# Optimization experiments

Hardware: AMD Instinct MI355X
Metric: run time of the kernel (lower is better)

## Reference

```python
import jax, jax.numpy as jnp
import numpy as np

HIDDEN = 512
N_HEAD = 8
D_HEAD = 64
MAX_REL = 3
B, S = 2, 2048


def setup_inputs() -> dict:
    key = jax.random.key(0)
    ks = jax.random.split(key, 12)
    sc = 1.0 / np.sqrt(HIDDEN)
    return {
        "query": jax.random.normal(ks[0], (B, S, HIDDEN), jnp.float32),
        "key_": jax.random.normal(ks[1], (B, S, HIDDEN), jnp.float32),
        "value": jax.random.normal(ks[2], (B, S, HIDDEN), jnp.float32),
        "mask": jnp.zeros((B, S, S), dtype=bool),
        "pos_matrix": jax.random.randint(ks[3], (S, S), 0, MAX_REL, jnp.int32),
        "Wq": jax.random.normal(ks[4], (HIDDEN, HIDDEN), jnp.float32) * sc,
        "bq": jnp.zeros((HIDDEN,), jnp.float32),
        "Wk": jax.random.normal(ks[5], (HIDDEN, HIDDEN), jnp.float32) * sc,
        "bk": jnp.zeros((HIDDEN,), jnp.float32),
        "Wv": jax.random.normal(ks[6], (HIDDEN, HIDDEN), jnp.float32) * sc,
        "bv": jnp.zeros((HIDDEN,), jnp.float32),
        "Wo": jax.random.normal(ks[7], (HIDDEN, HIDDEN), jnp.float32) * sc,
        "bo": jnp.zeros((HIDDEN,), jnp.float32),
        "rel_table": jax.random.normal(ks[8], (MAX_REL, D_HEAD), jnp.float32) * 0.1,
    }


def reference(query, key_, value, mask, pos_matrix, Wq, bq, Wk, bk, Wv, bv, Wo, bo, rel_table):
    b, s, hid = query.shape
    H, D = N_HEAD, D_HEAD
    q = (query @ Wq + bq).reshape(b, s, H, D)   # [B,S,H,D]
    k = (key_ @ Wk + bk).reshape(b, s, H, D)
    v = (value @ Wv + bv).reshape(b, s, H, D)
    rel = rel_table[pos_matrix[:s, :s]]          # [S,S,D]
    # attn1: content-content; attn2: q vs rel-pos; attn3: k(row) vs rel-pos
    attn1 = jnp.einsum('bihd,bjhd->bhij', q, k)
    attn2 = jnp.einsum('bihd,ijd->bhij', q, rel)
    attn3 = jnp.einsum('bihd,ijd->bhij', k, rel)
    scale = jnp.sqrt(jnp.asarray(D, query.dtype))
    attn = (attn1 + attn2 + attn3) / scale
    attn = jnp.where(mask[:, None, :, :], jnp.asarray(-1e9, attn.dtype), attn)
    attn = jax.nn.softmax(attn, axis=-1)         # dropout=0 (eval)
    x = jnp.einsum('bhij,bjhd->bihd', attn, v).reshape(b, s, hid)
    out = x @ Wo + bo
    return out, attn
```

## Files before the change

kernel.cpp:

```cpp
#include <hip/hip_runtime.h>
#include <math.h>

#define SEQ   2048
#define BATCH 2
#define NHEAD 8
#define HID   512
#define LG8   0.180336880f
#define MASKV -3.0e8f

typedef unsigned char  u8;
typedef unsigned short u16;
typedef short short8 __attribute__((ext_vector_type(8)));
typedef float f32x4  __attribute__((ext_vector_type(4)));

__device__ __forceinline__ u16 f2bf(float f) {
    unsigned u = __float_as_uint(f);
    u = (u + 0x7FFF + ((u >> 16) & 1)) >> 16;
    return (u16)u;
}
__device__ __forceinline__ float bf2f(u16 h) {
    return __uint_as_float(((unsigned)h) << 16);
}

__global__ __launch_bounds__(256) void gemm_bias_kernel(
    const float* __restrict__ A, const float* __restrict__ W,
    const float* __restrict__ bias, float* __restrict__ C, int M)
{
    __shared__ float As[16][68];
    __shared__ float Bs[16][64];
    const int tid = threadIdx.x;
    const int ty = tid >> 4, tx = tid & 15;
    const int row0 = blockIdx.x << 6;
    const int col0 = blockIdx.y << 6;
    const int am = tid >> 2, ak = (tid & 3) << 2;
    const int wk = tid >> 4, wn = (tid & 15) << 2;

    float acc[4][4] = {};
    for (int k0 = 0; k0 < HID; k0 += 16) {
        float4 a4 = *(const float4*)&A[(size_t)(row0 + am) * HID + k0 + ak];
        float4 w4 = *(const float4*)&W[(size_t)(k0 + wk) * HID + col0 + wn];
        __syncthreads();
        As[ak + 0][am] = a4.x; As[ak + 1][am] = a4.y;
        As[ak + 2][am] = a4.z; As[ak + 3][am] = a4.w;
        *(float4*)&Bs[wk][wn] = w4;
        __syncthreads();
        #pragma unroll
        for (int kk = 0; kk < 16; ++kk) {
            float4 a = *(const float4*)&As[kk][ty << 2];
            float4 w = *(const float4*)&Bs[kk][tx << 2];
            acc[0][0] += a.x * w.x; acc[0][1] += a.x * w.y; acc[0][2] += a.x * w.z; acc[0][3] += a.x * w.w;
            acc[1][0] += a.y * w.x; acc[1][1] += a.y * w.y; acc[1][2] += a.y * w.z; acc[1][3] += a.y * w.w;
            acc[2][0] += a.z * w.x; acc[2][1] += a.z * w.y; acc[2][2] += a.z * w.z; acc[2][3] += a.z * w.w;
            acc[3][0] += a.w * w.x; acc[3][1] += a.w * w.y; acc[3][2] += a.w * w.z; acc[3][3] += a.w * w.w;
        }
    }
    float4 bv = *(const float4*)&bias[col0 + (tx << 2)];
    #pragma unroll
    for (int i = 0; i < 4; ++i) {
        float4 o = { acc[i][0] + bv.x, acc[i][1] + bv.y, acc[i][2] + bv.z, acc[i][3] + bv.w };
        *(float4*)&C[(size_t)(row0 + (ty << 2) + i) * HID + col0 + (tx << 2)] = o;
    }
}

__global__ __launch_bounds__(256) void convert_qkv_kernel(
    const float* __restrict__ q, const float* __restrict__ k, const float* __restrict__ v,
    u16* __restrict__ qh, u16* __restrict__ ql,
    u16* __restrict__ kh, u16* __restrict__ kl, u16* __restrict__ vb)
{
    const size_t i = ((size_t)blockIdx.x * 256 + threadIdx.x) * 4;
    float4 qv = *(const float4*)&q[i];
    float4 kv = *(const float4*)&k[i];
    float4 vv = *(const float4*)&v[i];
    ushort4 oqh, oql, okh, okl, ovb;
    float s; u16 hh;
    s = qv.x * LG8; hh = f2bf(s); oqh.x = hh; oql.x = f2bf(s - bf2f(hh));
    s = qv.y * LG8; hh = f2bf(s); oqh.y = hh; oql.y = f2bf(s - bf2f(hh));
    s = qv.z * LG8; hh = f2bf(s); oqh.z = hh; oql.z = f2bf(s - bf2f(hh));
    s = qv.w * LG8; hh = f2bf(s); oqh.w = hh; oql.w = f2bf(s - bf2f(hh));
    s = kv.x;       hh = f2bf(s); okh.x = hh; okl.x = f2bf(s - bf2f(hh));
    s = kv.y;       hh = f2bf(s); okh.y = hh; okl.y = f2bf(s - bf2f(hh));
    s = kv.z;       hh = f2bf(s); okh.z = hh; okl.z = f2bf(s - bf2f(hh));
    s = kv.w;       hh = f2bf(s); okh.w = hh; okl.w = f2bf(s - bf2f(hh));
    ovb.x = f2bf(vv.x); ovb.y = f2bf(vv.y); ovb.z = f2bf(vv.z); ovb.w = f2bf(vv.w);
    *(ushort4*)&qh[i] = oqh; *(ushort4*)&ql[i] = oql;
    *(ushort4*)&kh[i] = okh; *(ushort4*)&kl[i] = okl;
    *(ushort4*)&vb[i] = ovb;
}

__global__ __launch_bounds__(256) void convert_pm_kernel(
    const int* __restrict__ pos, const u8* __restrict__ mask, u8* __restrict__ pm)
{
    const size_t s = ((size_t)blockIdx.x * 256 + threadIdx.x) * 4;
    int4  p = *(const int4*)&pos[s & (size_t)(SEQ * SEQ - 1)];
    uchar4 m = *(const uchar4*)&mask[s];
    uchar4 o;
    o.x = m.x ? (u8)3 : (u8)p.x;
    o.y = m.y ? (u8)3 : (u8)p.y;
    o.z = m.z ? (u8)3 : (u8)p.z;
    o.w = m.w ? (u8)3 : (u8)p.w;
    *(uchar4*)&pm[s] = o;
}

__global__ __launch_bounds__(256) void rel_dots_kernel(
    const float* __restrict__ q, const float* __restrict__ k,
    const float* __restrict__ rel_table, float* __restrict__ dqk)
{
    const int w = blockIdx.x * 4 + (threadIdx.x >> 6);
    const int lane = threadIdx.x & 63;
    const int h = w % NHEAD;
    const int is = w / NHEAD;
    const int b = is / SEQ;
    const int i = is % SEQ;
    const size_t base = (size_t)is * HID + h * 64 + lane;
    const float s = q[base] + k[base];
    float p0 = s * rel_table[lane];
    float p1 = s * rel_table[64 + lane];
    float p2 = s * rel_table[128 + lane];
    #pragma unroll
    for (int off = 32; off; off >>= 1) {
        p0 += __shfl_xor(p0, off);
        p1 += __shfl_xor(p1, off);
        p2 += __shfl_xor(p2, off);
    }
    if (lane == 0) {
        size_t o = (((size_t)b * NHEAD + h) * SEQ + i) << 2;
        dqk[o + 0] = p0 * LG8; dqk[o + 1] = p1 * LG8; dqk[o + 2] = p2 * LG8;
    }
}

__global__ __launch_bounds__(256) void attn_stats_kernel(
    const u16* __restrict__ qh, const u16* __restrict__ ql,
    const u16* __restrict__ kh, const u16* __restrict__ kl,
    const float* __restrict__ dqk, const u8* __restrict__ pm,
    float* __restrict__ invl)
{
    __shared__ __align__(16) u16 Kh[64 * 72];
    __shared__ __align__(16) u16 Kl[64 * 72];
    __shared__ __align__(16) u8  PM[64 * 64];
    __shared__ float Ds[64][4];
    const int tid = threadIdx.x;
    const int wave = tid >> 6, lane = tid & 63;
    const int quad = lane >> 4, l15 = lane & 15;
    const int b = blockIdx.z, h = blockIdx.y, i0 = blockIdx.x << 6;
    const size_t bh = (size_t)(b * NHEAD + h);

    {
        const int i = tid >> 2, r = tid & 3;
        Ds[i][r] = (r == 3) ? MASKV : dqk[((bh * SEQ + i0 + i) << 2) + r];
    }
    const int irow = (wave << 4) + l15;
    const size_t qbase = ((size_t)(b * SEQ + i0 + irow)) * HID + h * 64 + (quad << 3);
    const short8 aqh0 = *(const short8*)&qh[qbase];
    const short8 aqh1 = *(const short8*)&qh[qbase + 32];
    const short8 aql0 = *(const short8*)&ql[qbase];
    const short8 aql1 = *(const short8*)&ql[qbase + 32];

    float srow[4] = {0.f, 0.f, 0.f, 0.f};

    for (int jt = 0; jt < SEQ / 64; ++jt) {
        const int j0 = jt << 6;
        __syncthreads();
        {
            const int rr = tid >> 3, cc = (tid & 7) << 3;
            const size_t g = ((size_t)(b * SEQ + j0 + rr)) * HID + h * 64 + cc;
            *(short8*)&Kh[rr * 72 + cc] = *(const short8*)&kh[g];
            *(short8*)&Kl[rr * 72 + cc] = *(const short8*)&kl[g];
            const size_t g2 = g + (size_t)32 * HID;
            *(short8*)&Kh[(rr + 32) * 72 + cc] = *(const short8*)&kh[g2];
            *(short8*)&Kl[(rr + 32) * 72 + cc] = *(const short8*)&kl[g2];
        }
        {
            const int r = tid >> 2, c = (tid & 3) << 4;
            *(uint4*)&PM[r * 64 + c] =
                *(const uint4*)&pm[((size_t)b * SEQ + i0 + r) * SEQ + j0 + c];
        }
        __syncthreads();

        #pragma unroll
        for (int sub = 0; sub < 4; ++sub) {
            const int n = (sub << 4) + l15;
            const short8 bh0 = *(const short8*)&Kh[n * 72 + (quad << 3)];
            const short8 bh1 = *(const short8*)&Kh[n * 72 + 32 + (quad << 3)];
            const short8 bl0 = *(const short8*)&Kl[n * 72 + (quad << 3)];
            const short8 bl1 = *(const short8*)&Kl[n * 72 + 32 + (quad << 3)];
            f32x4 acc = {0.f, 0.f, 0.f, 0.f};
            acc = __builtin_amdgcn_mfma_f32_16x16x32_bf16(aqh0, bh0, acc, 0, 0, 0);
            acc = __builtin_amdgcn_mfma_f32_16x16x32_bf16(aqh1, bh1, acc, 0, 0, 0);
            acc = __builtin_amdgcn_mfma_f32_16x16x32_bf16(aql0, bh0, acc, 0, 0, 0);
            acc = __builtin_amdgcn_mfma_f32_16x16x32_bf16(aql1, bh1, acc, 0, 0, 0);
            acc = __builtin_amdgcn_mfma_f32_16x16x32_bf16(aqh0, bl0, acc, 0, 0, 0);
            acc = __builtin_amdgcn_mfma_f32_16x16x32_bf16(aqh1, bl1, acc, 0, 0, 0);
            #pragma unroll
            for (int r = 0; r < 4; ++r) {
                const int il = (wave << 4) + (quad << 2) + r;
                const u8 p = PM[il * 64 + (sub << 4) + l15];
                srow[r] += exp2f(acc[r] + Ds[il][p]);
            }
        }
    }
    #pragma unroll
    for (int r = 0; r < 4; ++r) {
        float s = srow[r];
        s += __shfl_xor(s, 1); s += __shfl_xor(s, 2);
        s += __shfl_xor(s, 4); s += __shfl_xor(s, 8);
        if (l15 == 0)
            invl[bh * SEQ + i0 + (wave << 4) + (quad << 2) + r] = 1.0f / s;
    }
}

__global__ __launch_bounds__(256) void attn_fused_kernel(
    const u16* __restrict__ qh, const u16* __restrict__ ql,
    const u16* __restrict__ kh, const u16* __restrict__ kl,
    const u16* __restrict__ vb, const float* __restrict__ dqk,
    const u8* __restrict__ pm, const float* __restrict__ invl,
    float* __restrict__ attn, float* __restrict__ x)
{
    __shared__ __align__(16) u16 Kh[64 * 72];
    __shared__ __align__(16) u16 Kl[64 * 72];
    __shared__ __align__(16) u16 VtT[64 * 72];
    __shared__ __align__(16) u16 Pst[4][16 * 72];
    __shared__ __align__(16) u8  PM[64 * 64];
    __shared__ float Ds[64][4];
    const int tid = threadIdx.x;
    const int wave = tid >> 6, lane = tid & 63;
    const int quad = lane >> 4, l15 = lane & 15;
    const int b = blockIdx.z, h = blockIdx.y, i0 = blockIdx.x << 6;
    const size_t bh = (size_t)(b * NHEAD + h);

    {
        const int i = tid >> 2, r = tid & 3;
        Ds[i][r] = (r == 3) ? MASKV : dqk[((bh * SEQ + i0 + i) << 2) + r];
    }
    float inv_r[4];
    #pragma unroll
    for (int r = 0; r < 4; ++r)
        inv_r[r] = invl[bh * SEQ + i0 + (wave << 4) + (quad << 2) + r];

    const int irow = (wave << 4) + l15;
    const size_t qbase = ((size_t)(b * SEQ + i0 + irow)) * HID + h * 64 + (quad << 3);
    const short8 aqh0 = *(const short8*)&qh[qbase];
    const short8 aqh1 = *(const short8*)&qh[qbase + 32];
    const short8 aql0 = *(const short8*)&ql[qbase];
    const short8 aql1 = *(const short8*)&ql[qbase + 32];

    f32x4 accX[4] = {{0.f,0.f,0.f,0.f},{0.f,0.f,0.f,0.f},{0.f,0.f,0.f,0.f},{0.f,0.f,0.f,0.f}};

    for (int jt = 0; jt < SEQ / 64; ++jt) {
        const int j0 = jt << 6;
        __syncthreads();
        {
            const int rr = tid >> 3, cc = (tid & 7) << 3;
            const size_t g = ((size_t)(b * SEQ + j0 + rr)) * HID + h * 64 + cc;
            *(short8*)&Kh[rr * 72 + cc] = *(const short8*)&kh[g];
            *(short8*)&Kl[rr * 72 + cc] = *(const short8*)&kl[g];
            const size_t g2 = g + (size_t)32 * HID;
            *(short8*)&Kh[(rr + 32) * 72 + cc] = *(const short8*)&kh[g2];
            *(short8*)&Kl[(rr + 32) * 72 + cc] = *(const short8*)&kl[g2];
        }
        {
            const int r = tid >> 2, c = (tid & 3) << 4;
            *(uint4*)&PM[r * 64 + c] =
                *(const uint4*)&pm[((size_t)b * SEQ + i0 + r) * SEQ + j0 + c];
        }
        {
            const int jr = tid & 63, d0 = (tid >> 6) << 4;
            const size_t g = ((size_t)(b * SEQ + j0 + jr)) * HID + h * 64 + d0;
            const short8 v0 = *(const short8*)&vb[g];
            const short8 v1 = *(const short8*)&vb[g + 8];
            #pragma unroll
            for (int e = 0; e < 8; ++e) {
                VtT[(d0 + e) * 72 + jr]     = (u16)v0[e];
                VtT[(d0 + 8 + e) * 72 + jr] = (u16)v1[e];
            }
        }
        __syncthreads();

        #pragma unroll
        for (int sub = 0; sub < 4; ++sub) {
            const int n = (sub << 4) + l15;
            const short8 bh0 = *(const short8*)&Kh[n * 72 + (quad << 3)];
            const short8 bh1 = *(const short8*)&Kh[n * 72 + 32 + (quad << 3)];
            const short8 bl0 = *(const short8*)&Kl[n * 72 + (quad << 3)];
            const short8 bl1 = *(const short8*)&Kl[n * 72 + 32 + (quad << 3)];
            f32x4 acc = {0.f, 0.f, 0.f, 0.f};
            acc = __builtin_amdgcn_mfma_f32_16x16x32_bf16(aqh0, bh0, acc, 0, 0, 0);
            acc = __builtin_amdgcn_mfma_f32_16x16x32_bf16(aqh1, bh1, acc, 0, 0, 0);
            acc = __builtin_amdgcn_mfma_f32_16x16x32_bf16(aql0, bh0, acc, 0, 0, 0);
            acc = __builtin_amdgcn_mfma_f32_16x16x32_bf16(aql1, bh1, acc, 0, 0, 0);
            acc = __builtin_amdgcn_mfma_f32_16x16x32_bf16(aqh0, bl0, acc, 0, 0, 0);
            acc = __builtin_amdgcn_mfma_f32_16x16x32_bf16(aqh1, bl1, acc, 0, 0, 0);
            #pragma unroll
            for (int r = 0; r < 4; ++r) {
                const int il = (wave << 4) + (quad << 2) + r;
                const u8 p = PM[il * 64 + (sub << 4) + l15];
                const float pr = exp2f(acc[r] + Ds[il][p]) * inv_r[r];
                attn[(bh * SEQ + i0 + il) * SEQ + j0 + (sub << 4) + l15] = pr;
                Pst[wave][((quad << 2) + r) * 72 + (sub << 4) + l15] = f2bf(pr);
            }
        }
        const short8 bp0 = *(const short8*)&Pst[wave][l15 * 72 + (quad << 3)];
        const short8 bp1 = *(const short8*)&Pst[wave][l15 * 72 + 32 + (quad << 3)];
        #pragma unroll
        for (int m = 0; m < 4; ++m) {
            const short8 av0 = *(const short8*)&VtT[((m << 4) + l15) * 72 + (quad << 3)];
            const short8 av1 = *(const short8*)&VtT[((m << 4) + l15) * 72 + 32 + (quad << 3)];
            accX[m] = __builtin_amdgcn_mfma_f32_16x16x32_bf16(av0, bp0, accX[m], 0, 0, 0);
            accX[m] = __builtin_amdgcn_mfma_f32_16x16x32_bf16(av1, bp1, accX[m], 0, 0, 0);
        }
    }
    const size_t xrow = ((size_t)(b * SEQ + i0 + (wave << 4) + l15)) * HID + h * 64;
    #pragma unroll
    for (int m = 0; m < 4; ++m) {
        *(f32x4*)&x[xrow + (m << 4) + (quad << 2)] = accX[m];
    }
}

extern "C" void kernel_launch(void* const* d_in, const int* in_sizes, int n_in,
                              void* d_out, int out_size, void* d_ws, size_t ws_size,
                              hipStream_t stream) {
    (void)in_sizes; (void)n_in; (void)out_size; (void)ws_size;
    const float* query = (const float*)d_in[0];
    const float* key_  = (const float*)d_in[1];
    const float* value = (const float*)d_in[2];
    const u8*    mask  = (const u8*)d_in[3];
    const int*   pos   = (const int*)d_in[4];
    const float* Wq = (const float*)d_in[5];
    const float* bq = (const float*)d_in[6];
    const float* Wk = (const float*)d_in[7];
    const float* bk = (const float*)d_in[8];
    const float* Wv = (const float*)d_in[9];
    const float* bv = (const float*)d_in[10];
    const float* Wo = (const float*)d_in[11];
    const float* bo = (const float*)d_in[12];
    const float* rel_table = (const float*)d_in[13];

    float* out  = (float*)d_out;
    float* attn = out + (size_t)BATCH * SEQ * HID;

    float* q_ws = (float*)d_ws;
    float* k_ws = q_ws + (size_t)2097152;
    float* v_ws = k_ws + (size_t)2097152;
    float* dqk  = v_ws + (size_t)2097152;
    float* invl = dqk + (size_t)131072;
    u16* qh = (u16*)(invl + 32768);
    u16* ql = qh + (size_t)2097152;
    u16* kh = ql + (size_t)2097152;
    u16* kl = kh + (size_t)2097152;
    u16* vb = kl + (size_t)2097152;
    u8*  pm = (u8*)(vb + (size_t)2097152);
    float* x_ws = q_ws;

    const dim3 blk(256);
    const int M = BATCH * SEQ;

    gemm_bias_kernel<<<dim3(M / 64, HID / 64), blk, 0, stream>>>(query, Wq, bq, q_ws, M);
    gemm_bias_kernel<<<dim3(M / 64, HID / 64), blk, 0, stream>>>(key_, Wk, bk, k_ws, M);
    gemm_bias_kernel<<<dim3(M / 64, HID / 64), blk, 0, stream>>>(value, Wv, bv, v_ws, M);
    rel_dots_kernel<<<dim3(BATCH * SEQ * NHEAD / 4), blk, 0, stream>>>(q_ws, k_ws, rel_table, dqk);
    convert_qkv_kernel<<<dim3(2048), blk, 0, stream>>>(q_ws, k_ws, v_ws, qh, ql, kh, kl, vb);
    convert_pm_kernel<<<dim3(8192), blk, 0, stream>>>(pos, mask, pm);
    attn_stats_kernel<<<dim3(SEQ / 64, NHEAD, BATCH), blk, 0, stream>>>(
        qh, ql, kh, kl, dqk, pm, invl);
    attn_fused_kernel<<<dim3(SEQ / 64, NHEAD, BATCH), blk, 0, stream>>>(
        qh, ql, kh, kl, vb, dqk, pm, invl, attn, x_ws);
    gemm_bias_kernel<<<dim3(M / 64, HID / 64), blk, 0, stream>>>(x_ws, Wo, bo, out, M);
}
```

Before: 673.0 us.

## Move projections to split-bf16 MFMA GEMMs and materialize exp scores for separate PV pass

The four fp32 SIMT projection GEMMs become MFMA GEMMs that use a hi/lo bf16 split of activations and pre-transposed weights, preceded by conversion kernels. The attention is split differently. The stats pass now also writes unnormalized bf16 exp scores to a full BxHxSxS workspace. A second pass reads those scores back, writes the normalized attn output and does PV with a pre-transposed V. This cuts redundant QK recomputation and moves GEMM work to matrix cores. In exchange it adds a large extra global write and read of the score matrix, extra conversion and transpose launches, and K loads that now come straight from global instead of LDS. The attn output is now computed from bf16-rounded exp values, which lowers its precision.

```diff
diff --git a/kernel.cpp b/kernel.cpp
--- a/kernel.cpp
+++ b/kernel.cpp
@@ -21,73 +21,62 @@
 __device__ __forceinline__ float bf2f(u16 h) {
     return __uint_as_float(((unsigned)h) << 16);
 }
-
-__global__ __launch_bounds__(256) void gemm_bias_kernel(
-    const float* __restrict__ A, const float* __restrict__ W,
-    const float* __restrict__ bias, float* __restrict__ C, int M)
-{
-    __shared__ float As[16][68];
-    __shared__ float Bs[16][64];
-    const int tid = threadIdx.x;
-    const int ty = tid >> 4, tx = tid & 15;
-    const int row0 = blockIdx.x << 6;
-    const int col0 = blockIdx.y << 6;
-    const int am = tid >> 2, ak = (tid & 3) << 2;
-    const int wk = tid >> 4, wn = (tid & 15) << 2;
-
-    float acc[4][4] = {};
-    for (int k0 = 0; k0 < HID; k0 += 16) {
-        float4 a4 = *(const float4*)&A[(size_t)(row0 + am) * HID + k0 + ak];
-        float4 w4 = *(const float4*)&W[(size_t)(k0 + wk) * HID + col0 + wn];
-        __syncthreads();
-        As[ak + 0][am] = a4.x; As[ak + 1][am] = a4.y;
-        As[ak + 2][am] = a4.z; As[ak + 3][am] = a4.w;
-        *(float4*)&Bs[wk][wn] = w4;
-        __syncthreads();
-        #pragma unroll
-        for (int kk = 0; kk < 16; ++kk) {
-            float4 a = *(const float4*)&As[kk][ty << 2];
-            float4 w = *(const float4*)&Bs[kk][tx << 2];
-            acc[0][0] += a.x * w.x; acc[0][1] += a.x * w.y; acc[0][2] += a.x * w.z; acc[0][3] += a.x * w.w;
-            acc[1][0] += a.y * w.x; acc[1][1] += a.y * w.y; acc[1][2] += a.y * w.z; acc[1][3] += a.y * w.w;
-            acc[2][0] += a.z * w.x; acc[2][1] += a.z * w.y; acc[2][2] += a.z * w.z; acc[2][3] += a.z * w.w;
-            acc[3][0] += a.w * w.x; acc[3][1] += a.w * w.y; acc[3][2] += a.w * w.z; acc[3][3] += a.w * w.w;
-        }
-    }
-    float4 bv = *(const float4*)&bias[col0 + (tx << 2)];
-    #pragma unroll
-    for (int i = 0; i < 4; ++i) {
-        float4 o = { acc[i][0] + bv.x, acc[i][1] + bv.y, acc[i][2] + bv.z, acc[i][3] + bv.w };
-        *(float4*)&C[(size_t)(row0 + (ty << 2) + i) * HID + col0 + (tx << 2)] = o;
-    }
-}
-
-__global__ __launch_bounds__(256) void convert_qkv_kernel(
+__device__ __forceinline__ void split2(float s, u16& h, u16& l) {
+    h = f2bf(s); l = f2bf(s - bf2f(h));
+}
+
+__global__ __launch_bounds__(256) void conv_act(
     const float* __restrict__ q, const float* __restrict__ k, const float* __restrict__ v,
-    u16* __restrict__ qh, u16* __restrict__ ql,
-    u16* __restrict__ kh, u16* __restrict__ kl, u16* __restrict__ vb)
+    u16* __restrict__ Qh, u16* __restrict__ Ql, u16* __restrict__ Kh, u16* __restrict__ Kl,
+    u16* __restrict__ Vh, u16* __restrict__ Vl)
 {
     const size_t i = ((size_t)blockIdx.x * 256 + threadIdx.x) * 4;
     float4 qv = *(const float4*)&q[i];
     float4 kv = *(const float4*)&k[i];
     float4 vv = *(const float4*)&v[i];
-    ushort4 oqh, oql, okh, okl, ovb;
-    float s; u16 hh;
-    s = qv.x * LG8; hh = f2bf(s); oqh.x = hh; oql.x = f2bf(s - bf2f(hh));
-    s = qv.y * LG8; hh = f2bf(s); oqh.y = hh; oql.y = f2bf(s - bf2f(hh));
-    s = qv.z * LG8; hh = f2bf(s); oqh.z = hh; oql.z = f2bf(s - bf2f(hh));
-    s = qv.w * LG8; hh = f2bf(s); oqh.w = hh; oql.w = f2bf(s - bf2f(hh));
-    s = kv.x;       hh = f2bf(s); okh.x = hh; okl.x = f2bf(s - bf2f(hh));
-    s = kv.y;       hh = f2bf(s); okh.y = hh; okl.y = f2bf(s - bf2f(hh));
-    s = kv.z;       hh = f2bf(s); okh.z = hh; okl.z = f2bf(s - bf2f(hh));
-    s = kv.w;       hh = f2bf(s); okh.w = hh; okl.w = f2bf(s - bf2f(hh));
-    ovb.x = f2bf(vv.x); ovb.y = f2bf(vv.y); ovb.z = f2bf(vv.z); ovb.w = f2bf(vv.w);
-    *(ushort4*)&qh[i] = oqh; *(ushort4*)&ql[i] = oql;
-    *(ushort4*)&kh[i] = okh; *(ushort4*)&kl[i] = okl;
-    *(ushort4*)&vb[i] = ovb;
-}
-
-__global__ __launch_bounds__(256) void convert_pm_kernel(
+    ushort4 a, b, c, d, e, f;
+    split2(qv.x, a.x, b.x); split2(qv.y, a.y, b.y); split2(qv.z, a.z, b.z); split2(qv.w, a.w, b.w);
+    split2(kv.x, c.x, d.x); split2(kv.y, c.y, d.y); split2(kv.z, c.z, d.z); split2(kv.w, c.w, d.w);
+    split2(vv.x, e.x, f.x); split2(vv.y, e.y, f.y); split2(vv.z, e.z, f.z); split2(vv.w, e.w, f.w);
+    *(ushort4*)&Qh[i] = a; *(ushort4*)&Ql[i] = b;
+    *(ushort4*)&Kh[i] = c; *(ushort4*)&Kl[i] = d;
+    *(ushort4*)&Vh[i] = e; *(ushort4*)&Vl[i] = f;
+}
+
+__global__ __launch_bounds__(256) void conv_w(
+    const float* __restrict__ W0, const float* __restrict__ W1,
+    const float* __restrict__ W2, const float* __restrict__ W3,
+    u16* __restrict__ wt)
+{
+    __shared__ float T[64][68];
+    const float* Wz = (blockIdx.z == 0) ? W0 : (blockIdx.z == 1) ? W1 : (blockIdx.z == 2) ? W2 : W3;
+    u16* wh = wt + (size_t)blockIdx.z * 2 * 262144;
+    u16* wl = wh + 262144;
+    const int t = threadIdx.x;
+    const int k0 = blockIdx.x << 6, n0 = blockIdx.y << 6;
+    {
+        const int r = t >> 2, c = (t & 3) << 4;
+        #pragma unroll
+        for (int cc = 0; cc < 16; cc += 4)
+            *(float4*)&T[r][c + cc] = *(const float4*)&Wz[(size_t)(k0 + r) * HID + n0 + c + cc];
+    }
+    __syncthreads();
+    {
+        const int n = t >> 2, kc = (t & 3) << 4;
+        short8 h0, l0, h1, l1;
+        #pragma unroll
+        for (int e = 0; e < 8; ++e) {
+            u16 hh, ll;
+            split2(T[kc + e][n], hh, ll);     h0[e] = (short)hh; l0[e] = (short)ll;
+            split2(T[kc + 8 + e][n], hh, ll); h1[e] = (short)hh; l1[e] = (short)ll;
+        }
+        const size_t o = (size_t)(n0 + n) * HID + k0 + kc;
+        *(short8*)&wh[o] = h0; *(short8*)&wh[o + 8] = h1;
+        *(short8*)&wl[o] = l0; *(short8*)&wl[o + 8] = l1;
+    }
+}
+
+__global__ __launch_bounds__(256) void conv_pm(
     const int* __restrict__ pos, const u8* __restrict__ mask, u8* __restrict__ pm)
 {
     const size_t s = ((size_t)blockIdx.x * 256 + threadIdx.x) * 4;
@@ -101,8 +90,84 @@
     *(uchar4*)&pm[s] = o;
 }
 
+template<int OMODE>
+__global__ __launch_bounds__(256) void gemm_mfma(
+    const u16* __restrict__ Ah, const u16* __restrict__ Al,
+    const u16* __restrict__ Wh, const u16* __restrict__ Wl,
+    const float* __restrict__ bias,
+    float* __restrict__ Cf, u16* __restrict__ Ch, u16* __restrict__ Cl)
+{
+    const int tid = threadIdx.x;
+    const int wave = tid >> 6, lane = tid & 63;
+    const int quad = lane >> 4, l15 = lane & 15;
+    const int row0 = blockIdx.x << 6, n0 = blockIdx.y << 6;
+    const size_t abase = (size_t)(row0 + (wave << 4) + l15) * HID + (quad << 3);
+
+    f32x4 acc[4] = {{0.f,0.f,0.f,0.f},{0.f,0.f,0.f,0.f},{0.f,0.f,0.f,0.f},{0.f,0.f,0.f,0.f}};
+    #pragma unroll 4
+    for (int k0 = 0; k0 < HID; k0 += 32) {
+        const short8 ah = *(const short8*)&Ah[abase + k0];
+        const short8 al = *(const short8*)&Al[abase + k0];
+        #pragma unroll
+        for (int nt = 0; nt < 4; ++nt) {
+            const size_t wb = (size_t)(n0 + (nt << 4) + l15) * HID + k0 + (quad << 3);
+            const short8 bh = *(const short8*)&Wh[wb];
+            const short8 bl = *(const short8*)&Wl[wb];
+            acc[nt] = __builtin_amdgcn_mfma_f32_16x16x32_bf16(ah, bh, acc[nt], 0, 0, 0);
+            acc[nt] = __builtin_amdgcn_mfma_f32_16x16x32_bf16(al, bh, acc[nt], 0, 0, 0);
+            acc[nt] = __builtin_amdgcn_mfma_f32_16x16x32_bf16(ah, bl, acc[nt], 0, 0, 0);
+        }
+    }
+    #pragma unroll
+    for (int nt = 0; nt < 4; ++nt) {
+        const int col = n0 + (nt << 4) + l15;
+        const float bv = bias[col];
+        #pragma unroll
+        for (int r = 0; r < 4; ++r) {
+            const size_t idx = (size_t)(row0 + (wave << 4) + (quad << 2) + r) * HID + col;
+            const float v = acc[nt][r] + bv;
+            if (OMODE == 0) {
+                Cf[idx] = v;
+            } else if (OMODE == 1) {
+                u16 hh, ll; split2(v, hh, ll);
+                Ch[idx] = hh; Cl[idx] = ll;
+            } else {
+                Ch[idx] = f2bf(v);
+            }
+        }
+    }
+}
+
+__global__ __launch_bounds__(256) void transpose_v(
+    const u16* __restrict__ vb, u16* __restrict__ vt)
+{
+    __shared__ u16 T[64][72];
+    const int t = threadIdx.x;
+    const int j0 = blockIdx.x << 6, bhh = blockIdx.y;
+    const int b = bhh >> 3, h = bhh & 7;
+    {
+        const int r = t >> 2, c = (t & 3) << 4;
+        const size_t g = (size_t)(b * SEQ + j0 + r) * HID + h * 64 + c;
+        *(short8*)&T[r][c]     = *(const short8*)&vb[g];
+        *(short8*)&T[r][c + 8] = *(const short8*)&vb[g + 8];
+    }
+    __syncthreads();
+    {
+        const int d = t >> 2, jc = (t & 3) << 4;
+        short8 o0, o1;
+        #pragma unroll
+        for (int e = 0; e < 8; ++e) {
+            o0[e] = (short)T[jc + e][d];
+            o1[e] = (short)T[jc + 8 + e][d];
+        }
+        const size_t o = ((size_t)bhh * 64 + d) * SEQ + j0 + jc;
+        *(short8*)&vt[o] = o0; *(short8*)&vt[o + 8] = o1;
+    }
+}
+
 __global__ __launch_bounds__(256) void rel_dots_kernel(
-    const float* __restrict__ q, const float* __restrict__ k,
+    const u16* __restrict__ qh, const u16* __restrict__ ql,
+    const u16* __restrict__ kh, const u16* __restrict__ kl,
     const float* __restrict__ rel_table, float* __restrict__ dqk)
 {
     const int w = blockIdx.x * 4 + (threadIdx.x >> 6);
@@ -112,7 +177,7 @@
     const int b = is / SEQ;
     const int i = is % SEQ;
     const size_t base = (size_t)is * HID + h * 64 + lane;
-    const float s = q[base] + k[base];
+    const float s = (bf2f(qh[base]) + bf2f(ql[base])) + (bf2f(kh[base]) + bf2f(kl[base]));
     float p0 = s * rel_table[lane];
     float p1 = s * rel_table[64 + lane];
     float p2 = s * rel_table[128 + lane];
@@ -128,16 +193,14 @@
     }
 }
 
-__global__ __launch_bounds__(256) void attn_stats_kernel(
+__global__ __launch_bounds__(256) void attn_exp(
     const u16* __restrict__ qh, const u16* __restrict__ ql,
     const u16* __restrict__ kh, const u16* __restrict__ kl,
     const float* __restrict__ dqk, const u8* __restrict__ pm,
-    float* __restrict__ invl)
-{
-    __shared__ __align__(16) u16 Kh[64 * 72];
-    __shared__ __align__(16) u16 Kl[64 * 72];
-    __shared__ __align__(16) u8  PM[64 * 64];
+    u16* __restrict__ Pt, float* __restrict__ invl)
+{
     __shared__ float Ds[64][4];
+    __shared__ __align__(16) u16 Pst[4][16 * 72];
     const int tid = threadIdx.x;
     const int wave = tid >> 6, lane = tid & 63;
     const int quad = lane >> 4, l15 = lane & 15;
@@ -148,41 +211,26 @@
         const int i = tid >> 2, r = tid & 3;
         Ds[i][r] = (r == 3) ? MASKV : dqk[((bh * SEQ + i0 + i) << 2) + r];
     }
-    const int irow = (wave << 4) + l15;
-    const size_t qbase = ((size_t)(b * SEQ + i0 + irow)) * HID + h * 64 + (quad << 3);
+    __syncthreads();
+
+    const size_t qbase = ((size_t)(b * SEQ + i0 + (wave << 4) + l15)) * HID + h * 64 + (quad << 3);
     const short8 aqh0 = *(const short8*)&qh[qbase];
     const short8 aqh1 = *(const short8*)&qh[qbase + 32];
     const short8 aql0 = *(const short8*)&ql[qbase];
     const short8 aql1 = *(const short8*)&ql[qbase + 32];
 
+    const size_t prow = ((size_t)bh * SEQ + i0 + (wave << 4)) * SEQ;
     float srow[4] = {0.f, 0.f, 0.f, 0.f};
 
     for (int jt = 0; jt < SEQ / 64; ++jt) {
         const int j0 = jt << 6;
-        __syncthreads();
-        {
-            const int rr = tid >> 3, cc = (tid & 7) << 3;
-            const size_t g = ((size_t)(b * SEQ + j0 + rr)) * HID + h * 64 + cc;
-            *(short8*)&Kh[rr * 72 + cc] = *(const short8*)&kh[g];
-            *(short8*)&Kl[rr * 72 + cc] = *(const short8*)&kl[g];
-            const size_t g2 = g + (size_t)32 * HID;
-            *(short8*)&Kh[(rr + 32) * 72 + cc] = *(const short8*)&kh[g2];
-            *(short8*)&Kl[(rr + 32) * 72 + cc] = *(const short8*)&kl[g2];
-        }
-        {
-            const int r = tid >> 2, c = (tid & 3) << 4;
-            *(uint4*)&PM[r * 64 + c] =
-                *(const uint4*)&pm[((size_t)b * SEQ + i0 + r) * SEQ + j0 + c];
-        }
-        __syncthreads();
-
         #pragma unroll
         for (int sub = 0; sub < 4; ++sub) {
-            const int n = (sub << 4) + l15;
-            const short8 bh0 = *(const short8*)&Kh[n * 72 + (quad << 3)];
-            const short8 bh1 = *(const short8*)&Kh[n * 72 + 32 + (quad << 3)];
-            const short8 bl0 = *(const short8*)&Kl[n * 72 + (quad << 3)];
-            const short8 bl1 = *(const short8*)&Kl[n * 72 + 32 + (quad << 3)];
+            const size_t kb = ((size_t)(b * SEQ + j0 + (sub << 4) + l15)) * HID + h * 64 + (quad << 3);
+            const short8 bh0 = *(const short8*)&kh[kb];
+            const short8 bh1 = *(const short8*)&kh[kb + 32];
+            const short8 bl0 = *(const short8*)&kl[kb];
+            const short8 bl1 = *(const short8*)&kl[kb + 32];
             f32x4 acc = {0.f, 0.f, 0.f, 0.f};
             acc = __builtin_amdgcn_mfma_f32_16x16x32_bf16(aqh0, bh0, acc, 0, 0, 0);
             acc = __builtin_amdgcn_mfma_f32_16x16x32_bf16(aqh1, bh1, acc, 0, 0, 0);
@@ -193,10 +241,16 @@
             #pragma unroll
             for (int r = 0; r < 4; ++r) {
                 const int il = (wave << 4) + (quad << 2) + r;
-                const u8 p = PM[il * 64 + (sub << 4) + l15];
-                srow[r] += exp2f(acc[r] + Ds[il][p]);
+                const u8 p = pm[(size_t)b * SEQ * SEQ + (size_t)(i0 + il) * SEQ + j0 + (sub << 4) + l15];
+                const float e = exp2f(fmaf(acc[r], LG8, Ds[il][p]));
+                srow[r] += e;
+                Pst[wave][((quad << 2) + r) * 72 + (sub << 4) + l15] = f2bf(e);
             }
         }
+        const short8 p0 = *(const short8*)&Pst[wave][l15 * 72 + (quad << 4)];
+        const short8 p1 = *(const short8*)&Pst[wave][l15 * 72 + (quad << 4) + 8];
+        *(short8*)&Pt[prow + (size_t)l15 * SEQ + j0 + (quad << 4)]     = p0;
+        *(short8*)&Pt[prow + (size_t)l15 * SEQ + j0 + (quad << 4) + 8] = p1;
     }
     #pragma unroll
     for (int r = 0; r < 4; ++r) {
@@ -208,110 +262,64 @@
     }
 }
 
-__global__ __launch_bounds__(256) void attn_fused_kernel(
-    const u16* __restrict__ qh, const u16* __restrict__ ql,
-    const u16* __restrict__ kh, const u16* __restrict__ kl,
-    const u16* __restrict__ vb, const float* __restrict__ dqk,
-    const u8* __restrict__ pm, const float* __restrict__ invl,
-    float* __restrict__ attn, float* __restrict__ x)
-{
-    __shared__ __align__(16) u16 Kh[64 * 72];
-    __shared__ __align__(16) u16 Kl[64 * 72];
-    __shared__ __align__(16) u16 VtT[64 * 72];
-    __shared__ __align__(16) u16 Pst[4][16 * 72];
-    __shared__ __align__(16) u8  PM[64 * 64];
-    __shared__ float Ds[64][4];
+__global__ __launch_bounds__(256) void attn_pv2(
+    const u16* __restrict__ Pt, const u16* __restrict__ vt,
+    const float* __restrict__ invl,
+    float* __restrict__ attn, u16* __restrict__ xh, u16* __restrict__ xl)
+{
+    __shared__ __align__(16) u16 Ps[4][16 * 72];
     const int tid = threadIdx.x;
     const int wave = tid >> 6, lane = tid & 63;
     const int quad = lane >> 4, l15 = lane & 15;
     const int b = blockIdx.z, h = blockIdx.y, i0 = blockIdx.x << 6;
     const size_t bh = (size_t)(b * NHEAD + h);
 
-    {
-        const int i = tid >> 2, r = tid & 3;
-        Ds[i][r] = (r == 3) ? MASKV : dqk[((bh * SEQ + i0 + i) << 2) + r];
-    }
-    float inv_r[4];
-    #pragma unroll
-    for (int r = 0; r < 4; ++r)
-        inv_r[r] = invl[bh * SEQ + i0 + (wave << 4) + (quad << 2) + r];
-
-    const int irow = (wave << 4) + l15;
-    const size_t qbase = ((size_t)(b * SEQ + i0 + irow)) * HID + h * 64 + (quad << 3);
-    const short8 aqh0 = *(const short8*)&qh[qbase];
-    const short8 aqh1 = *(const short8*)&qh[qbase + 32];
-    const short8 aql0 = *(const short8*)&ql[qbase];
-    const short8 aql1 = *(const short8*)&ql[qbase + 32];
+    const int rloc = lane >> 2;
+    const int cloc = (lane & 3) << 4;
+    const int grow = i0 + (wave << 4) + rloc;
+    const float inv = invl[bh * SEQ + grow];
+    const size_t prow = ((size_t)bh * SEQ + grow) * SEQ;
 
     f32x4 accX[4] = {{0.f,0.f,0.f,0.f},{0.f,0.f,0.f,0.f},{0.f,0.f,0.f,0.f},{0.f,0.f,0.f,0.f}};
 
     for (int jt = 0; jt < SEQ / 64; ++jt) {
         const int j0 = jt << 6;
-        __syncthreads();
-        {
-            const int rr = tid >> 3, cc = (tid & 7) << 3;
-            const size_t g = ((size_t)(b * SEQ + j0 + rr)) * HID + h * 64 + cc;
-            *(short8*)&Kh[rr * 72 + cc] = *(const short8*)&kh[g];
-            *(short8*)&Kl[rr * 72 + cc] = *(const short8*)&kl[g];
-            const size_t g2 = g + (size_t)32 * HID;
-            *(short8*)&Kh[(rr + 32) * 72 + cc] = *(const short8*)&kh[g2];
-            *(short8*)&Kl[(rr + 32) * 72 + cc] = *(const short8*)&kl[g2];
-        }
-        {
-            const int r = tid >> 2, c = (tid & 3) << 4;
-            *(uint4*)&PM[r * 64 + c] =
-                *(const uint4*)&pm[((size_t)b * SEQ + i0 + r) * SEQ + j0 + c];
-        }
-        {
-            const int jr = tid & 63, d0 = (tid >> 6) << 4;
-            const size_t g = ((size_t)(b * SEQ + j0 + jr)) * HID + h * 64 + d0;
-            const short8 v0 = *(const short8*)&vb[g];
-            const short8 v1 = *(const short8*)&vb[g + 8];
+        const short8 t0 = *(const short8*)&Pt[prow + j0 + cloc];
+        const short8 t1 = *(const short8*)&Pt[prow + j0 + cloc + 8];
+        float4 o0 = { bf2f((u16)t0[0]) * inv, bf2f((u16)t0[1]) * inv, bf2f((u16)t0[2]) * inv, bf2f((u16)t0[3]) * inv };
+        float4 o1 = { bf2f((u16)t0[4]) * inv, bf2f((u16)t0[5]) * inv, bf2f((u16)t0[6]) * inv, bf2f((u16)t0[7]) * inv };
+        float4 o2 = { bf2f((u16)t1[0]) * inv, bf2f((u16)t1[1]) * inv, bf2f((u16)t1[2]) * inv, bf2f((u16)t1[3]) * inv };
+        float4 o3 = { bf2f((u16)t1[4]) * inv, bf2f((u16)t1[5]) * inv, bf2f((u16)t1[6]) * inv, bf2f((u16)t1[7]) * inv };
+        *(float4*)&attn[prow + j0 + cloc + 0]  = o0;
+        *(float4*)&attn[prow + j0 + cloc + 4]  = o1;
+        *(float4*)&attn[prow + j0 + cloc + 8]  = o2;
+        *(float4*)&attn[prow + j0 + cloc + 12] = o3;
+        *(short8*)&Ps[wave][rloc * 72 + cloc]     = t0;
+        *(short8*)&Ps[wave][rloc * 72 + cloc + 8] = t1;
+        #pragma unroll
+        for (int kk = 0; kk < 2; ++kk) {
+            const short8 ap = *(const short8*)&Ps[wave][l15 * 72 + (kk << 5) + (quad << 3)];
             #pragma unroll
-            for (int e = 0; e < 8; ++e) {
-                VtT[(d0 + e) * 72 + jr]     = (u16)v0[e];
-                VtT[(d0 + 8 + e) * 72 + jr] = (u16)v1[e];
+            for (int nt = 0; nt < 4; ++nt) {
+                const short8 bv = *(const short8*)&vt[((size_t)bh * 64 + (nt << 4) + l15) * SEQ + j0 + (kk << 5) + (quad << 3)];
+                accX[nt] = __builtin_amdgcn_mfma_f32_16x16x32_bf16(ap, bv, accX[nt], 0, 0, 0);
             }
         }
-        __syncthreads();
-
-        #pragma unroll
-        for (int sub = 0; sub < 4; ++sub) {
-            const int n = (sub << 4) + l15;
-            const short8 bh0 = *(const short8*)&Kh[n * 72 + (quad << 3)];
-            const short8 bh1 = *(const short8*)&Kh[n * 72 + 32 + (quad << 3)];
-            const short8 bl0 = *(const short8*)&Kl[n * 72 + (quad << 3)];
-            const short8 bl1 = *(const short8*)&Kl[n * 72 + 32 + (quad << 3)];
-            f32x4 acc = {0.f, 0.f, 0.f, 0.f};
-            acc = __builtin_amdgcn_mfma_f32_16x16x32_bf16(aqh0, bh0, acc, 0, 0, 0);
-            acc = __builtin_amdgcn_mfma_f32_16x16x32_bf16(aqh1, bh1, acc, 0, 0, 0);
-            acc = __builtin_amdgcn_mfma_f32_16x16x32_bf16(aql0, bh0, acc, 0, 0, 0);
-            acc = __builtin_amdgcn_mfma_f32_16x16x32_bf16(aql1, bh1, acc, 0, 0, 0);
-            acc = __builtin_amdgcn_mfma_f32_16x16x32_bf16(aqh0, bl0, acc, 0, 0, 0);
-            acc = __builtin_amdgcn_mfma_f32_16x16x32_bf16(aqh1, bl1, acc, 0, 0, 0);
-            #pragma unroll
-            for (int r = 0; r < 4; ++r) {
-                const int il = (wave << 4) + (quad << 2) + r;
-                const u8 p = PM[il * 64 + (sub << 4) + l15];
-                const float pr = exp2f(acc[r] + Ds[il][p]) * inv_r[r];
-                attn[(bh * SEQ + i0 + il) * SEQ + j0 + (sub << 4) + l15] = pr;
-                Pst[wave][((quad << 2) + r) * 72 + (sub << 4) + l15] = f2bf(pr);
-            }
-        }
-        const short8 bp0 = *(const short8*)&Pst[wave][l15 * 72 + (quad << 3)];
-        const short8 bp1 = *(const short8*)&Pst[wave][l15 * 72 + 32 + (quad << 3)];
-        #pragma unroll
-        for (int m = 0; m < 4; ++m) {
-            const short8 av0 = *(const short8*)&VtT[((m << 4) + l15) * 72 + (quad << 3)];
-            const short8 av1 = *(const short8*)&VtT[((m << 4) + l15) * 72 + 32 + (quad << 3)];
-            accX[m] = __builtin_amdgcn_mfma_f32_16x16x32_bf16(av0, bp0, accX[m], 0, 0, 0);
-            accX[m] = __builtin_amdgcn_mfma_f32_16x16x32_bf16(av1, bp1, accX[m], 0, 0, 0);
-        }
-    }
-    const size_t xrow = ((size_t)(b * SEQ + i0 + (wave << 4) + l15)) * HID + h * 64;
-    #pragma unroll
-    for (int m = 0; m < 4; ++m) {
-        *(f32x4*)&x[xrow + (m << 4) + (quad << 2)] = accX[m];
+    }
+    float invr[4];
+    #pragma unroll
+    for (int r = 0; r < 4; ++r)
+        invr[r] = invl[bh * SEQ + i0 + (wave << 4) + (quad << 2) + r];
+    #pragma unroll
+    for (int nt = 0; nt < 4; ++nt) {
+        #pragma unroll
+        for (int r = 0; r < 4; ++r) {
+            const float v = accX[nt][r] * invr[r];
+            const size_t idx = (size_t)(b * SEQ + i0 + (wave << 4) + (quad << 2) + r) * HID
+                             + h * 64 + (nt << 4) + l15;
+            u16 hh, ll; split2(v, hh, ll);
+            xh[idx] = hh; xl[idx] = ll;
+        }
     }
 }
 
@@ -337,31 +345,45 @@
     float* out  = (float*)d_out;
     float* attn = out + (size_t)BATCH * SEQ * HID;
 
-    float* q_ws = (float*)d_ws;
-    float* k_ws = q_ws + (size_t)2097152;
-    float* v_ws = k_ws + (size_t)2097152;
-    float* dqk  = v_ws + (size_t)2097152;
-    float* invl = dqk + (size_t)131072;
-    u16* qh = (u16*)(invl + 32768);
-    u16* ql = qh + (size_t)2097152;
-    u16* kh = ql + (size_t)2097152;
-    u16* kl = kh + (size_t)2097152;
-    u16* vb = kl + (size_t)2097152;
-    u8*  pm = (u8*)(vb + (size_t)2097152);
-    float* x_ws = q_ws;
+    const size_t NE = (size_t)BATCH * SEQ * HID;
+    u16* w = (u16*)d_ws;
+    u16* qh  = w; w += NE;   u16* ql  = w; w += NE;
+    u16* kh  = w; w += NE;   u16* kl  = w; w += NE;
+    u16* vb  = w; w += NE;
+    u16* Qih = w; w += NE;   u16* Qil = w; w += NE;
+    u16* Kih = w; w += NE;   u16* Kil = w; w += NE;
+    u16* Vih = w; w += NE;   u16* Vil = w; w += NE;
+    u16* xh  = w; w += NE;   u16* xl  = w; w += NE;
+    u16* vt  = w; w += NE;
+    u16* wt  = w; w += (size_t)4 * 2 * 262144;
+    u16* Pt  = w; w += (size_t)BATCH * NHEAD * SEQ * SEQ;
+    float* dqk  = (float*)w;
+    float* invl = dqk + (size_t)BATCH * NHEAD * SEQ * 4;
+    u8*    pm   = (u8*)(invl + (size_t)BATCH * NHEAD * SEQ);
 
     const dim3 blk(256);
     const int M = BATCH * SEQ;
 
-    gemm_bias_kernel<<<dim3(M / 64, HID / 64), blk, 0, stream>>>(query, Wq, bq, q_ws, M);
-    gemm_bias_kernel<<<dim3(M / 64, HID / 64), blk, 0, stream>>>(key_, Wk, bk, k_ws, M);
-    gemm_bias_kernel<<<dim3(M / 64, HID / 64), blk, 0, stream>>>(value, Wv, bv, v_ws, M);
-    rel_dots_kernel<<<dim3(BATCH * SEQ * NHEAD / 4), blk, 0, stream>>>(q_ws, k_ws, rel_table, dqk);
-    convert_qkv_kernel<<<dim3(2048), blk, 0, stream>>>(q_ws, k_ws, v_ws, qh, ql, kh, kl, vb);
-    convert_pm_kernel<<<dim3(8192), blk, 0, stream>>>(pos, mask, pm);
-    attn_stats_kernel<<<dim3(SEQ / 64, NHEAD, BATCH), blk, 0, stream>>>(
-        qh, ql, kh, kl, dqk, pm, invl);
-    attn_fused_kernel<<<dim3(SEQ / 64, NHEAD, BATCH), blk, 0, stream>>>(
-        qh, ql, kh, kl, vb, dqk, pm, invl, attn, x_ws);
-    gemm_bias_kernel<<<dim3(M / 64, HID / 64), blk, 0, stream>>>(x_ws, Wo, bo, out, M);
-}
+    conv_act<<<dim3(2048), blk, 0, stream>>>(query, key_, value, Qih, Qil, Kih, Kil, Vih, Vil);
+    conv_w<<<dim3(8, 8, 4), blk, 0, stream>>>(Wq, Wk, Wv, Wo, wt);
+    conv_pm<<<dim3(8192), blk, 0, stream>>>(pos, mask, pm);
+
+    u16* wtq = wt;            u16* wtk = wt + 2 * 262144;
+    u16* wtv = wt + 4 * 262144; u16* wto = wt + 6 * 262144;
+    gemm_mfma<1><<<dim3(M / 64, HID / 64), blk, 0, stream>>>(
+        Qih, Qil, wtq, wtq + 262144, bq, nullptr, qh, ql);
+    gemm_mfma<1><<<dim3(M / 64, HID / 64), blk, 0, stream>>>(
+        Kih, Kil, wtk, wtk + 262144, bk, nullptr, kh, kl);
+    gemm_mfma<2><<<dim3(M / 64, HID / 64), blk, 0, stream>>>(
+        Vih, Vil, wtv, wtv + 262144, bv, nullptr, vb, nullptr);
+    transpose_v<<<dim3(SEQ / 64, BATCH * NHEAD), blk, 0, stream>>>(vb, vt);
+    rel_dots_kernel<<<dim3(M * NHEAD / 4), blk, 0, stream>>>(qh, ql, kh, kl, rel_table, dqk);
+
+    attn_exp<<<dim3(SEQ / 64, NHEAD, BATCH), blk, 0, stream>>>(
+        qh, ql, kh, kl, dqk, pm, Pt, invl);
+    attn_pv2<<<dim3(SEQ / 64, NHEAD, BATCH), blk, 0, stream>>>(
+        Pt, vt, invl, attn, xh, xl);
+
+    gemm_mfma<0><<<dim3(M / 64, HID / 64), blk, 0, stream>>>(
+        xh, xl, wto, wto + 262144, bo, out, nullptr, nullptr);
+}
```

Result: slower. 775.4 us (+15.2%).
